# Optimization experiments

Measured on AMD Instinct MI355X. Metric: run time of the kernel, lower is better.

Reference implementation:

```python
import jax, jax.numpy as jnp
import numpy as np

B, LQ, LC, LN, D, H = 4, 1024, 1024, 1024, 1024, 16
HD = D // H
LS_INIT = 1e-4
RES_MAX = 10.0
EPS = 1e-5


def layernorm(x, g, b):
    mu = jnp.mean(x, axis=-1, keepdims=True)
    var = jnp.var(x, axis=-1, keepdims=True)
    return (x - mu) * jax.lax.rsqrt(var + EPS) * g + b


def setup_inputs() -> dict:
    key = jax.random.key(0)
    ks = jax.random.split(key, 12)
    s = 0.02
    return {
        "tight_tokens": jax.random.normal(ks[0], (B, LQ, D), jnp.float32),
        "context_tokens": jax.random.normal(ks[1], (B, LC, D), jnp.float32),
        "neighborhood_tokens": jax.random.normal(ks[2], (B, LN, D), jnp.float32),
        "ln_q_g": jnp.ones((D,), jnp.float32), "ln_q_b": jnp.zeros((D,), jnp.float32),
        "ln_kv_g": jnp.ones((D,), jnp.float32), "ln_kv_b": jnp.zeros((D,), jnp.float32),
        "in_proj_w": jax.random.normal(ks[3], (3 * D, D), jnp.float32) * s,
        "in_proj_b": jnp.zeros((3 * D,), jnp.float32),
        "out_proj_w": jax.random.normal(ks[4], (D, D), jnp.float32) * s,
        "out_proj_b": jnp.zeros((D,), jnp.float32),
        "cross_gamma": jnp.full((D,), LS_INIT, jnp.float32),
        "ln_f_g": jnp.ones((D,), jnp.float32), "ln_f_b": jnp.zeros((D,), jnp.float32),
        "w1": jax.random.normal(ks[5], (4 * D, D), jnp.float32) * s,
        "b1": jnp.zeros((4 * D,), jnp.float32),
        "w2": jax.random.normal(ks[6], (D, 4 * D), jnp.float32) * s,
        "b2": jnp.zeros((D,), jnp.float32),
        "ffn_gamma": jnp.full((D,), LS_INIT, jnp.float32),
    }


def reference(tight_tokens, context_tokens, neighborhood_tokens,
              ln_q_g, ln_q_b, ln_kv_g, ln_kv_b,
              in_proj_w, in_proj_b, out_proj_w, out_proj_b, cross_gamma,
              ln_f_g, ln_f_b, w1, b1, w2, b2, ffn_gamma):
    kv = jnp.concatenate([context_tokens, neighborhood_tokens], axis=1)  # [B, LKV, D]
    q_in = layernorm(tight_tokens, ln_q_g, ln_q_b)
    kv_in = layernorm(kv, ln_kv_g, ln_kv_b)

    wq, wk, wv = jnp.split(in_proj_w, 3, axis=0)
    bq, bk, bv = jnp.split(in_proj_b, 3, axis=0)
    q = (q_in @ wq.T + bq).reshape(B, LQ, H, HD)
    k = (kv_in @ wk.T + bk).reshape(B, -1, H, HD)
    v = (kv_in @ wv.T + bv).reshape(B, -1, H, HD)

    scores = jnp.einsum('bqhd,bkhd->bhqk', q, k) / jnp.sqrt(jnp.float32(HD))
    attn = jax.nn.softmax(scores, axis=-1)  # [B, H, LQ, LKV]
    ctx = jnp.einsum('bhqk,bkhd->bqhd', attn, v).reshape(B, LQ, D)
    attn_out = ctx @ out_proj_w.T + out_proj_b

    cg = jnp.clip(cross_gamma, -RES_MAX, RES_MAX)
    x = tight_tokens + attn_out * cg

    h = layernorm(x, ln_f_g, ln_f_b)
    h = jax.nn.gelu(h @ w1.T + b1, approximate=False) @ w2.T + b2
    fg = jnp.clip(ffn_gamma, -RES_MAX, RES_MAX)
    x = x + h * fg

    return x, attn.mean(axis=1)
```

## Files before the change

kernel.cpp:

```cpp
#include <hip/hip_runtime.h>
#include <math.h>

typedef unsigned short u16;
typedef __attribute__((ext_vector_type(8))) short bf16x8;
typedef __attribute__((ext_vector_type(4))) float f32x4;

#define MFMA16(a,b,c) __builtin_amdgcn_mfma_f32_16x16x32_bf16(a,b,c,0,0,0)

__device__ __forceinline__ u16 f2bf(float f){
  union { float f; unsigned int u; } x; x.f = f;
  unsigned int r = x.u + 0x7fffu + ((x.u >> 16) & 1u);
  return (u16)(r >> 16);
}

__device__ __forceinline__ void gload16(const void* g, void* lds){
  __builtin_amdgcn_global_load_lds(
    (const __attribute__((address_space(1))) unsigned int*)g,
    (__attribute__((address_space(3))) unsigned int*)lds, 16, 0, 0);
}

__global__ __launch_bounds__(256) void cvt_weights(
    const float* __restrict__ wqkv, const float* __restrict__ wo,
    const float* __restrict__ w1, const float* __restrict__ w2,
    u16* __restrict__ o0, u16* __restrict__ o1,
    u16* __restrict__ o2, u16* __restrict__ o3)
{
  int idx = blockIdx.x * 256 + threadIdx.x;
  const float* src; u16* dst;
  if (idx < 786432)                    { src = wqkv; dst = o0; }
  else if ((idx -= 786432) < 262144)   { src = wo;   dst = o1; }
  else if ((idx -= 262144) < 1048576)  { src = w1;   dst = o2; }
  else { idx -= 1048576;                 src = w2;   dst = o3; }
  float4 v = ((const float4*)src)[idx];
  short4 o;
  o.x = (short)f2bf(v.x); o.y = (short)f2bf(v.y);
  o.z = (short)f2bf(v.z); o.w = (short)f2bf(v.w);
  ((short4*)dst)[idx] = o;
}

template<int MODE>
__global__ __launch_bounds__(256) void ln_kernel(
    const float* __restrict__ s0, const float* __restrict__ s1,
    const float* __restrict__ g, const float* __restrict__ be,
    u16* __restrict__ out)
{
  int row = blockIdx.x, t = threadIdx.x;
  const float* src;
  if (MODE == 1) {
    int b = row >> 11, p = row & 2047;
    src = (p < 1024) ? s0 + ((long)(b*1024 + p))*1024
                     : s1 + ((long)(b*1024 + p - 1024))*1024;
  } else {
    src = s0 + (long)row * 1024;
  }
  float4 v = ((const float4*)src)[t];
  float s  = v.x + v.y + v.z + v.w;
  float ss = v.x*v.x + v.y*v.y + v.z*v.z + v.w*v.w;
  #pragma unroll
  for (int m = 1; m < 64; m <<= 1) { s += __shfl_xor(s, m); ss += __shfl_xor(ss, m); }
  __shared__ float red[8];
  int l = t & 63, w = t >> 6;
  if (l == 0) { red[w*2] = s; red[w*2+1] = ss; }
  __syncthreads();
  s  = red[0] + red[2] + red[4] + red[6];
  ss = red[1] + red[3] + red[5] + red[7];
  float mean = s * (1.0f/1024.0f);
  float var  = ss * (1.0f/1024.0f) - mean*mean;
  float rstd = rsqrtf(var + 1e-5f);
  float4 gv = ((const float4*)g)[t];
  float4 bv = ((const float4*)be)[t];
  short4 o;
  o.x = (short)f2bf((v.x-mean)*rstd*gv.x + bv.x);
  o.y = (short)f2bf((v.y-mean)*rstd*gv.y + bv.y);
  o.z = (short)f2bf((v.z-mean)*rstd*gv.z + bv.z);
  o.w = (short)f2bf((v.w-mean)*rstd*gv.w + bv.w);
  *(short4*)(out + (long)row*1024 + t*4) = o;
}

template<int EPI, int BM>
__global__ __launch_bounds__(256,2) void gemm_bt(
    const u16* __restrict__ A, const u16* __restrict__ Bt,
    int M, int N, int K,
    const float* __restrict__ bias,
    const float* __restrict__ gamma,
    const float* __restrict__ resid,
    float* __restrict__ outf,
    u16* __restrict__ outb0, u16* __restrict__ outb1)
{
  constexpr int MI = BM / 32;
  __shared__ __align__(16) u16 at[2][BM*64];
  __shared__ __align__(16) u16 bt[2][128*64];
  int nwg = gridDim.x;
  int bidx = (blockIdx.x & 7) * (nwg >> 3) + (blockIdx.x >> 3);
  int nb = N >> 7;
  int tm = bidx / nb, tn = bidx % nb;
  int m0 = tm * BM, n0 = tn << 7;
  int t = threadIdx.x, l = t & 63, w = t >> 6;
  int wr = (w >> 1) * (BM/2), wc = (w & 1) * 64;
  int fr = l & 15, fq = l >> 4;
  f32x4 acc[MI][4] = {};
  int rr = t >> 3;
  int cb = (t & 7) << 4;
  const char* Ab = (const char*)A;
  const char* Bp = (const char*)Bt;
  long ld = (long)K * 2;

#define G_STAGE(s, kt) do {                                                        \
    _Pragma("unroll")                                                              \
    for (int c = 0; c < MI; c++) {                                                 \
      int row = c*32 + rr;                                                         \
      gload16(Ab + (long)(m0 + row)*ld + (long)(kt)*2 + (cb ^ ((row & 7) << 4)),   \
              (char*)at[s] + c*4096 + w*1024);                                     \
    }                                                                              \
    _Pragma("unroll")                                                              \
    for (int c = 0; c < 4; c++) {                                                  \
      int row = c*32 + rr;                                                         \
      gload16(Bp + (long)(n0 + row)*ld + (long)(kt)*2 + (cb ^ ((row & 7) << 4)),   \
              (char*)bt[s] + c*4096 + w*1024);                                     \
    }                                                                              \
  } while (0)

  G_STAGE(0, 0);
  __syncthreads();
  int cur = 0;
  for (int kt = 0; kt < K; kt += 64) {
    if (kt + 64 < K) G_STAGE(cur ^ 1, kt + 64);
    #pragma unroll
    for (int ka = 0; ka < 2; ka++) {
      bf16x8 af[MI], bfv[4];
      #pragma unroll
      for (int i = 0; i < MI; i++) {
        int ra = wr + i*16 + fr;
        af[i] = *(const bf16x8*)((const char*)at[cur] + ra*128 + ((ka*64 + fq*16) ^ ((ra & 7) << 4)));
      }
      #pragma unroll
      for (int j = 0; j < 4; j++) {
        int rb = wc + j*16 + fr;
        bfv[j] = *(const bf16x8*)((const char*)bt[cur] + rb*128 + ((ka*64 + fq*16) ^ ((rb & 7) << 4)));
      }
      #pragma unroll
      for (int i = 0; i < MI; i++)
        #pragma unroll
        for (int j = 0; j < 4; j++)
          acc[i][j] = MFMA16(af[i], bfv[j], acc[i][j]);
    }
    __syncthreads();
    cur ^= 1;
  }
#undef G_STAGE
  #pragma unroll
  for (int i = 0; i < MI; i++) {
    #pragma unroll
    for (int j = 0; j < 4; j++) {
      #pragma unroll
      for (int r = 0; r < 4; r++) {
        int row = m0 + wr + i*16 + fq*4 + r;
        int col = n0 + wc + j*16 + fr;
        float v = acc[i][j][r];
        if constexpr (EPI == 0) {
          float qv = (v + bias[col]) * 0.18033688011112042f;
          int b = row >> 10, lq = row & 1023, h = col >> 6, hd = col & 63;
          outb0[(((long)(b*16 + h)) << 16) + (lq << 6) + hd] = f2bf(qv);
        } else if constexpr (EPI == 2) {
          float gs = gamma[col]; gs = fminf(fmaxf(gs, -10.f), 10.f);
          long idx = (long)row*1024 + col;
          outf[idx] = resid[idx] + (v + bias[col]) * gs;
        } else if constexpr (EPI == 3) {
          float u = v + bias[col];
          float ge = 0.5f * u * (1.0f + erff(u * 0.70710678118654752f));
          outb0[(long)row*4096 + col] = f2bf(ge);
        } else {
          float gs = gamma[col]; gs = fminf(fmaxf(gs, -10.f), 10.f);
          long idx = (long)row*1024 + col;
          outf[idx] = resid[idx] + (v + bias[col]) * gs;
        }
      }
    }
  }
}

template<int EPI>
__global__ __launch_bounds__(512, 2) void gemm256(
    const u16* __restrict__ A, const u16* __restrict__ Bt,
    int M, int N, int K,
    const float* __restrict__ bias,
    u16* __restrict__ outb0, u16* __restrict__ outb1)
{
  __shared__ __align__(16) u16 As[2][256*64];
  __shared__ __align__(16) u16 Bs[2][256*64];
  int nwg = gridDim.x;
  int bidx = (blockIdx.x & 7) * (nwg >> 3) + (blockIdx.x >> 3);
  int nb = N >> 8;
  int tm = bidx / nb, tn = bidx % nb;
  int m0 = tm << 8, n0 = tn << 8;
  int t = threadIdx.x, l = t & 63, w = t >> 6;
  int wm = w >> 2, wn = w & 3;
  int fr = l & 15, fq = l >> 4;
  int sr = t >> 3;
  int scb = (t & 7) << 4;
  int s7 = (sr & 7) << 4;
  const char* Ab = (const char*)A;
  const char* Bp = (const char*)Bt;
  long ld = (long)K * 2;

#define STAGE_AQ(slot, kt, q) do {                                               \
    int grow = (sr < 32) ? ((q)*32 + sr) : (128 + (q)*32 + sr - 32);             \
    int abase = (w < 4) ? ((q)*32 + w*8) : (128 + (q)*32 + (w - 4)*8);           \
    gload16(Ab + (long)(m0 + grow)*ld + (long)(kt)*2 + (scb ^ s7),               \
            (char*)As[slot] + abase*128);                                        \
  } while (0)
#define STAGE_BH(slot, kt, h) do {                                               \
    int r0 = (h)*128 + sr;                                                       \
    gload16(Bp + (long)(n0 + r0)*ld + (long)(kt)*2 + (scb ^ s7),                 \
            (char*)Bs[slot] + ((h)*128 + w*8)*128);                              \
    gload16(Bp + (long)(n0 + r0 + 64)*ld + (long)(kt)*2 + (scb ^ s7),            \
            (char*)Bs[slot] + ((h)*128 + 64 + w*8)*128);                         \
  } while (0)

  f32x4 acc[8][4] = {};
  int NT = K >> 6;

  STAGE_BH(0, 0, 0); STAGE_BH(0, 0, 1);
  STAGE_AQ(0, 0, 0); STAGE_AQ(0, 0, 1); STAGE_AQ(0, 0, 2); STAGE_AQ(0, 0, 3);
  STAGE_BH(1, 64, 0); STAGE_BH(1, 64, 1);
  asm volatile("s_waitcnt vmcnt(4)" ::: "memory");
  __builtin_amdgcn_s_barrier();
  asm volatile("" ::: "memory");

#define MFMA_PHASE(mibase)                                                       \
    __builtin_amdgcn_s_setprio(1);                                               \
    _Pragma("unroll")                                                            \
    for (int nj = 0; nj < 4; nj++) {                                             \
      acc[(mibase)][nj]   = MFMA16(a00, bfr[nj][0], acc[(mibase)][nj]);          \
      acc[(mibase)][nj]   = MFMA16(a01, bfr[nj][1], acc[(mibase)][nj]);          \
      acc[(mibase)+1][nj] = MFMA16(a10, bfr[nj][0], acc[(mibase)+1][nj]);        \
      acc[(mibase)+1][nj] = MFMA16(a11, bfr[nj][1], acc[(mibase)+1][nj]);        \
    }                                                                            \
    __builtin_amdgcn_s_setprio(0);

#define READ_A(p)                                                                \
    int r0_ = wm*128 + (2*(p))*16 + fr;                                          \
    int r1_ = r0_ + 16;                                                          \
    bf16x8 a00 = *(const bf16x8*)(Ab_s + r0_*128 + ((fq*16) ^ ((r0_ & 7) << 4)));        \
    bf16x8 a01 = *(const bf16x8*)(Ab_s + r0_*128 + ((64 + fq*16) ^ ((r0_ & 7) << 4)));   \
    bf16x8 a10 = *(const bf16x8*)(Ab_s + r1_*128 + ((fq*16) ^ ((r1_ & 7) << 4)));        \
    bf16x8 a11 = *(const bf16x8*)(Ab_s + r1_*128 + ((64 + fq*16) ^ ((r1_ & 7) << 4)));

  for (int tt = 0; tt < NT; tt++) {
    int s = tt & 1;
    const char* Ab_s = (const char*)As[s];
    const char* Bb_s = (const char*)Bs[s];
    int kt1 = (tt + 1) << 6, kt2 = (tt + 2) << 6;
    bf16x8 bfr[4][2];
    {
      #pragma unroll
      for (int nj = 0; nj < 4; nj++) {
        int rb = wn*64 + nj*16 + fr;
        bfr[nj][0] = *(const bf16x8*)(Bb_s + rb*128 + ((fq*16) ^ ((rb & 7) << 4)));
        bfr[nj][1] = *(const bf16x8*)(Bb_s + rb*128 + ((64 + fq*16) ^ ((rb & 7) << 4)));
      }
      READ_A(0)
      if (tt + 1 < NT) { STAGE_AQ(s ^ 1, kt1, 0); STAGE_AQ(s ^ 1, kt1, 1); }
      asm volatile("s_waitcnt lgkmcnt(8)" ::: "memory");
      __builtin_amdgcn_s_barrier();
      asm volatile("s_waitcnt lgkmcnt(0)" ::: "memory");
      MFMA_PHASE(0)
      __builtin_amdgcn_s_barrier();
    }
    {
      READ_A(1)
      if (tt + 1 < NT) { STAGE_AQ(s ^ 1, kt1, 2); STAGE_AQ(s ^ 1, kt1, 3); }
      __builtin_amdgcn_s_barrier();
      asm volatile("s_waitcnt lgkmcnt(0)" ::: "memory");
      MFMA_PHASE(2)
      __builtin_amdgcn_s_barrier();
    }
    {
      READ_A(2)
      if (tt + 2 < NT) STAGE_BH(s, kt2, 0);
      __builtin_amdgcn_s_barrier();
      asm volatile("s_waitcnt lgkmcnt(0)" ::: "memory");
      MFMA_PHASE(4)
      __builtin_amdgcn_s_barrier();
    }
    {
      READ_A(3)
      if (tt + 2 < NT) STAGE_BH(s, kt2, 1);
      __builtin_amdgcn_s_barrier();
      asm volatile("s_waitcnt lgkmcnt(0)" ::: "memory");
      MFMA_PHASE(6)
      if (tt + 1 < NT) {
        if (tt + 2 < NT) { asm volatile("s_waitcnt vmcnt(4)" ::: "memory"); }
        else             { asm volatile("s_waitcnt vmcnt(0)" ::: "memory"); }
      }
      __builtin_amdgcn_s_barrier();
      asm volatile("" ::: "memory");
    }
  }
#undef READ_A
#undef MFMA_PHASE
#undef STAGE_AQ
#undef STAGE_BH

  #pragma unroll
  for (int mi = 0; mi < 8; mi++) {
    #pragma unroll
    for (int nj = 0; nj < 4; nj++) {
      #pragma unroll
      for (int r = 0; r < 4; r++) {
        int row = m0 + wm*128 + mi*16 + fq*4 + r;
        int col = n0 + wn*64 + nj*16 + fr;
        float v = acc[mi][nj][r];
        if constexpr (EPI == 1) {
          float u = v + bias[col];
          int b = row >> 11, p = row & 2047;
          if (col < 1024) {
            int h = col >> 6, hd = col & 63;
            outb0[(((long)((b*16 + h)*2048 + p)) << 6) + hd] = f2bf(u);
          } else {
            int c2 = col - 1024, h = c2 >> 6, hd = c2 & 63;
            outb1[(((long)((b*16 + h)*64 + hd)) << 11) + p] = f2bf(u);
          }
        } else {
          float u = v + bias[col];
          float ge = 0.5f * u * (1.0f + erff(u * 0.70710678118654752f));
          outb0[(long)row*4096 + col] = f2bf(ge);
        }
      }
    }
  }
}

__global__ __launch_bounds__(256, 3) void flash_fwd(
    const u16* __restrict__ q, const u16* __restrict__ k,
    const u16* __restrict__ vt, u16* __restrict__ ctx,
    float* __restrict__ ilout)
{
  __shared__ __align__(16) u16 ks[2][64*64];
  __shared__ __align__(16) u16 vs[2][64*64];
  __shared__ __align__(16) char ps[4*4096];
  int nwg = gridDim.x;
  int bid = (blockIdx.x & 7) * (nwg >> 3) + (blockIdx.x >> 3);
  int qt = bid & 7, h = (bid >> 3) & 15, b = bid >> 7;
  int q0 = qt << 7;
  int t = threadIdx.x, l = t & 63, w = t >> 6;
  int fr = l & 15, fq = l >> 4;
  const char* qb = (const char*)(q  + (((long)(b*16 + h)) << 16));
  const char* kb = (const char*)(k  + (((long)(b*16 + h)) << 17));
  const char* vb = (const char*)(vt + (((long)(b*16 + h)) << 17));
  char* psw = ps + w*4096;
  int rr = t >> 3;
  int sc = (t & 7) << 4;

  #pragma unroll
  for (int c = 0; c < 2; c++) {
    int row = c*32 + rr;
    gload16(kb + (long)row*128 + (sc ^ ((row & 7) << 4)), (char*)ks[0] + c*4096 + w*1024);
    gload16(vb + (long)row*4096 + (sc ^ ((row & 7) << 4)), (char*)vs[0] + c*4096 + w*1024);
  }
  {
    int qr = l >> 3;
    #pragma unroll
    for (int c = 0; c < 4; c++) {
      int row = c*8 + qr;
      gload16(qb + (long)(q0 + w*32 + row)*128 + (sc ^ ((row & 7) << 4)), psw + c*1024);
    }
  }
  asm volatile("s_waitcnt vmcnt(0)" ::: "memory");
  bf16x8 qf[2][2];
  #pragma unroll
  for (int rf = 0; rf < 2; rf++) {
    int row = rf*16 + fr;
    qf[rf][0] = *(const bf16x8*)(psw + row*128 + ((fq*16) ^ ((row & 7) << 4)));
    qf[rf][1] = *(const bf16x8*)(psw + row*128 + ((64 + fq*16) ^ ((row & 7) << 4)));
  }
  asm volatile("s_waitcnt lgkmcnt(0)" ::: "memory");
  __builtin_amdgcn_s_barrier();
  asm volatile("" ::: "memory");

  f32x4 cacc[2][4] = {};
  f32x4 lrun[2] = {{0.f,0.f,0.f,0.f},{0.f,0.f,0.f,0.f}};
  int cur = 0;
  for (int kt = 0; kt < 2048; kt += 64) {
    int notlast = (kt + 64 < 2048);
    if (notlast) {
      #pragma unroll
      for (int c = 0; c < 2; c++) {
        int row = c*32 + rr;
        gload16(vb + (long)row*4096 + (long)(kt + 64)*2 + (sc ^ ((row & 7) << 4)),
                (char*)vs[cur ^ 1] + c*4096 + w*1024);
        gload16(kb + (long)(kt + 64 + row)*128 + (sc ^ ((row & 7) << 4)),
                (char*)ks[cur ^ 1] + c*4096 + w*1024);
      }
    }
    __builtin_amdgcn_sched_barrier(0);
    const char* ksb = (const char*)ks[cur];
    f32x4 sf[2][4];
    __builtin_amdgcn_s_setprio(1);
    #pragma unroll
    for (int cf = 0; cf < 4; cf++) {
      int row = cf*16 + fr;
      bf16x8 kf0 = *(const bf16x8*)(ksb + row*128 + ((fq*16) ^ ((row & 7) << 4)));
      bf16x8 kf1 = *(const bf16x8*)(ksb + row*128 + ((64 + fq*16) ^ ((row & 7) << 4)));
      #pragma unroll
      for (int rf = 0; rf < 2; rf++) {
        f32x4 a = {};
        a = MFMA16(qf[rf][0], kf0, a);
        sf[rf][cf] = MFMA16(qf[rf][1], kf1, a);
      }
    }
    __builtin_amdgcn_s_setprio(0);
    #pragma unroll
    for (int rf = 0; rf < 2; rf++)
      #pragma unroll
      for (int cf = 0; cf < 4; cf++)
        #pragma unroll
        for (int r = 0; r < 4; r++) {
          float pv = exp2f(sf[rf][cf][r]);
          lrun[rf][r] += pv;
          union { float f; unsigned int u; } pu; pu.f = pv;
          int prow = rf*16 + fq*4 + r;
          *(u16*)(psw + prow*128 + (((cf*16 + fr) << 1) ^ ((prow & 7) << 4))) = (u16)(pu.u >> 16);
        }
    bf16x8 pa[2][2];
    #pragma unroll
    for (int rf = 0; rf < 2; rf++) {
      int row = rf*16 + fr;
      pa[rf][0] = *(const bf16x8*)(psw + row*128 + ((fq*16) ^ ((row & 7) << 4)));
      pa[rf][1] = *(const bf16x8*)(psw + row*128 + ((64 + fq*16) ^ ((row & 7) << 4)));
    }
    __builtin_amdgcn_s_setprio(1);
    #pragma unroll
    for (int cfd = 0; cfd < 4; cfd++) {
      int hd = cfd*16 + fr;
      bf16x8 vf0 = *(const bf16x8*)((const char*)vs[cur] + hd*128 + ((fq*16) ^ ((hd & 7) << 4)));
      bf16x8 vf1 = *(const bf16x8*)((const char*)vs[cur] + hd*128 + ((64 + fq*16) ^ ((hd & 7) << 4)));
      #pragma unroll
      for (int rf = 0; rf < 2; rf++) {
        cacc[rf][cfd] = MFMA16(pa[rf][0], vf0, cacc[rf][cfd]);
        cacc[rf][cfd] = MFMA16(pa[rf][1], vf1, cacc[rf][cfd]);
      }
    }
    __builtin_amdgcn_s_setprio(0);
    if (notlast) {
      asm volatile("s_waitcnt vmcnt(0)" ::: "memory");
      __builtin_amdgcn_s_barrier();
      asm volatile("" ::: "memory");
    }
    cur ^= 1;
  }
  #pragma unroll
  for (int rf = 0; rf < 2; rf++) {
    float il4[4];
    #pragma unroll
    for (int r = 0; r < 4; r++) {
      float s = lrun[rf][r];
      #pragma unroll
      for (int msk = 1; msk < 16; msk <<= 1) s += __shfl_xor(s, msk, 16);
      il4[r] = 1.0f / s;
    }
    #pragma unroll
    for (int cf = 0; cf < 4; cf++)
      #pragma unroll
      for (int r = 0; r < 4; r++) {
        int row = q0 + w*32 + rf*16 + fq*4 + r;
        int col = h*64 + cf*16 + fr;
        ctx[(long)(b*1024 + row)*1024 + col] = f2bf(cacc[rf][cf][r] * il4[r]);
      }
    if (fr == 0) {
      #pragma unroll
      for (int r = 0; r < 4; r++) {
        int row = q0 + w*32 + rf*16 + fq*4 + r;
        long idx = (((long)(b*16 + h)) << 10) + row;
        ilout[idx] = il4[r];
      }
    }
  }
}

__global__ __launch_bounds__(256,2) void attn_mean(
    const u16* __restrict__ q, const u16* __restrict__ k,
    const float* __restrict__ il,
    float* __restrict__ out)
{
  __shared__ __align__(16) u16 qs[2][128*64];
  __shared__ __align__(16) u16 ks[2][128*64];
  __shared__ __align__(16) float ml[2][128];
  int nwg = gridDim.x;
  int bid = (blockIdx.x & 7) * (nwg >> 3) + (blockIdx.x >> 3);
  int kt = bid & 15, qt = (bid >> 4) & 7, b = bid >> 7;
  int q0 = qt << 7, k0 = kt << 7;
  int t = threadIdx.x, l = t & 63, w = t >> 6;
  int wr = (w >> 1) << 6, wc = (w & 1) << 6;
  int fr = l & 15, fq = l >> 4;
  int rr = t >> 3, cbb = (t & 7) << 4;
  const long bh = (long)b * 16;

#define AM_STAGE(hh, s) do {                                                        \
    const char* qb_ = (const char*)(q + ((bh + (hh)) << 16)) + (long)q0*128;        \
    const char* kb_ = (const char*)(k + ((bh + (hh)) << 17)) + (long)k0*128;        \
    _Pragma("unroll")                                                               \
    for (int c = 0; c < 4; c++) {                                                   \
      int row = c*32 + rr;                                                          \
      int sw = cbb ^ ((row & 7) << 4);                                              \
      gload16(qb_ + (long)row*128 + sw, (char*)qs[s] + c*4096 + w*1024);            \
      gload16(kb_ + (long)row*128 + sw, (char*)ks[s] + c*4096 + w*1024);            \
    }                                                                               \
    if (w == 0 && l < 32) {                                                         \
      gload16((const char*)(il + ((bh + (hh)) << 10) + q0) + l*16, (char*)ml[s]);   \
    }                                                                               \
  } while (0)

  AM_STAGE(0, 0);
  asm volatile("s_waitcnt vmcnt(0)" ::: "memory");
  __builtin_amdgcn_s_barrier();
  asm volatile("" ::: "memory");

  f32x4 macc[4][4] = {};
  for (int h = 0; h < 16; h++) {
    int cur = h & 1;
    if (h < 15) AM_STAGE(h + 1, cur ^ 1);
    const char* qsb = (const char*)qs[cur];
    const char* ksb = (const char*)ks[cur];
    const float* mlb = ml[cur];
    f32x4 ir4[4];
    #pragma unroll
    for (int i = 0; i < 4; i++)
      ir4[i] = *(const f32x4*)(mlb + wr + i*16 + fq*4);
    bf16x8 af[4][2], bf[4][2];
    #pragma unroll
    for (int i = 0; i < 4; i++) {
      int ra = wr + i*16 + fr;
      int rb = wc + i*16 + fr;
      af[i][0] = *(const bf16x8*)(qsb + ra*128 + ((fq*16) ^ ((ra & 7) << 4)));
      af[i][1] = *(const bf16x8*)(qsb + ra*128 + ((64 + fq*16) ^ ((ra & 7) << 4)));
      bf[i][0] = *(const bf16x8*)(ksb + rb*128 + ((fq*16) ^ ((rb & 7) << 4)));
      bf[i][1] = *(const bf16x8*)(ksb + rb*128 + ((64 + fq*16) ^ ((rb & 7) << 4)));
    }
    #pragma unroll
    for (int j = 0; j < 4; j++) {
      f32x4 sf[4];
      __builtin_amdgcn_s_setprio(1);
      #pragma unroll
      for (int i = 0; i < 4; i++) {
        f32x4 a = MFMA16(af[i][0], bf[j][0], {});
        sf[i] = MFMA16(af[i][1], bf[j][1], a);
      }
      __builtin_amdgcn_s_setprio(0);
      #pragma unroll
      for (int i = 0; i < 4; i++)
        #pragma unroll
        for (int r = 0; r < 4; r++)
          macc[i][j][r] += exp2f(sf[i][r]) * ir4[i][r];
    }
    asm volatile("s_waitcnt vmcnt(0)" ::: "memory");
    __builtin_amdgcn_s_barrier();
    asm volatile("" ::: "memory");
  }
#undef AM_STAGE
  #pragma unroll
  for (int i = 0; i < 4; i++)
    #pragma unroll
    for (int j = 0; j < 4; j++)
      #pragma unroll
      for (int r = 0; r < 4; r++) {
        int row = q0 + wr + i*16 + fq*4 + r;
        int col = k0 + wc + j*16 + fr;
        out[((long)(b*1024 + row) << 11) + col] = macc[i][j][r] * 0.0625f;
      }
}

extern "C" void kernel_launch(void* const* d_in, const int* in_sizes, int n_in,
                              void* d_out, int out_size, void* d_ws, size_t ws_size,
                              hipStream_t stream)
{
  (void)in_sizes; (void)n_in; (void)out_size; (void)ws_size;
  const float* tight = (const float*)d_in[0];
  const float* ctxt  = (const float*)d_in[1];
  const float* nbh   = (const float*)d_in[2];
  const float* lnqg  = (const float*)d_in[3];
  const float* lnqb  = (const float*)d_in[4];
  const float* lnkg  = (const float*)d_in[5];
  const float* lnkb  = (const float*)d_in[6];
  const float* wqkv  = (const float*)d_in[7];
  const float* bqkv  = (const float*)d_in[8];
  const float* wo    = (const float*)d_in[9];
  const float* bo    = (const float*)d_in[10];
  const float* cg    = (const float*)d_in[11];
  const float* lnfg  = (const float*)d_in[12];
  const float* lnfb  = (const float*)d_in[13];
  const float* w1    = (const float*)d_in[14];
  const float* b1    = (const float*)d_in[15];
  const float* w2    = (const float*)d_in[16];
  const float* b2    = (const float*)d_in[17];
  const float* fg    = (const float*)d_in[18];

  char* p = (char*)d_ws;
  u16* wqkv_bf = (u16*)p; p += 3072L*1024*2;
  u16* wo_bf   = (u16*)p; p += 1024L*1024*2;
  u16* w1_bf   = (u16*)p; p += 4096L*1024*2;
  u16* w2_bf   = (u16*)p; p += 1024L*4096*2;
  u16* qin_bf  = (u16*)p; p += 4096L*1024*2;
  u16* kvin_bf = (u16*)p; p += 8192L*1024*2;
  u16* q_bf    = (u16*)p; p += 4L*16*1024*64*2;
  u16* k_bf    = (u16*)p; p += 4L*16*2048*64*2;
  u16* vt_bf   = (u16*)p; p += 4L*16*64*2048*2;
  u16* ctx_bf  = (u16*)p; p += 4096L*1024*2;
  float* il_f  = (float*)p; p += 4L*16*1024*4;
  float* x_f   = (float*)p; p += 4096L*1024*4;
  u16* hln_bf  = (u16*)p; p += 4096L*1024*2;
  u16* gelu_bf = (u16*)p; p += 4096L*4096*2;

  float* x_out    = (float*)d_out;
  float* mean_out = x_out + 4194304;

  cvt_weights<<<12288, 256, 0, stream>>>(wqkv, wo, w1, w2, wqkv_bf, wo_bf, w1_bf, w2_bf);
  ln_kernel<0><<<4096, 256, 0, stream>>>(tight, nullptr, lnqg, lnqb, qin_bf);
  ln_kernel<1><<<8192, 256, 0, stream>>>(ctxt, nbh, lnkg, lnkb, kvin_bf);
  gemm_bt<0,64><<<512, 256, 0, stream>>>(qin_bf, wqkv_bf, 4096, 1024, 1024,
                                      bqkv, nullptr, nullptr, nullptr, q_bf, nullptr);
  gemm256<1><<<256, 512, 0, stream>>>(kvin_bf, wqkv_bf + 1024L*1024, 8192, 2048, 1024,
                                      bqkv + 1024, k_bf, vt_bf);
  flash_fwd<<<512, 256, 0, stream>>>(q_bf, k_bf, vt_bf, ctx_bf, il_f);
  attn_mean<<<512, 256, 0, stream>>>(q_bf, k_bf, il_f, mean_out);
  gemm_bt<2,64><<<512, 256, 0, stream>>>(ctx_bf, wo_bf, 4096, 1024, 1024,
                                      bo, cg, tight, x_f, nullptr, nullptr);
  ln_kernel<0><<<4096, 256, 0, stream>>>(x_f, nullptr, lnfg, lnfb, hln_bf);
  gemm256<3><<<256, 512, 0, stream>>>(hln_bf, w1_bf, 4096, 4096, 1024,
                                      b1, gelu_bf, nullptr);
  gemm_bt<4,64><<<512, 256, 0, stream>>>(gelu_bf, w2_bf, 4096, 1024, 4096,
                                      b2, fg, x_f, x_out, nullptr, nullptr);
}
```

Measured before the change: 360.6 us.

## Merge Q and KV projections into one launch; co-schedule attn-mean with out-proj

Replaces the separate Q-projection gemm_bt and KV gemm256 launches with a single 320-block gemm256_qkv that routes each block to the KV or Q tile by index. It also fuses the attention-mean kernel and the output-projection GEMM into one post_attn launch whose blocks branch between the two independent jobs. The aim is to cut launch overhead and tail underutilisation by filling the GPU with concurrent independent work. The cost is heterogeneous blocks inside one grid, with possible load imbalance, and a shared LDS footprint sized for the larger branch, which may lower occupancy.

```diff
diff --git a/kernel.cpp b/kernel.cpp
--- a/kernel.cpp
+++ b/kernel.cpp
@@ -157,15 +157,7 @@
         int row = m0 + wr + i*16 + fq*4 + r;
         int col = n0 + wc + j*16 + fr;
         float v = acc[i][j][r];
-        if constexpr (EPI == 0) {
-          float qv = (v + bias[col]) * 0.18033688011112042f;
-          int b = row >> 10, lq = row & 1023, h = col >> 6, hd = col & 63;
-          outb0[(((long)(b*16 + h)) << 16) + (lq << 6) + hd] = f2bf(qv);
-        } else if constexpr (EPI == 2) {
-          float gs = gamma[col]; gs = fminf(fmaxf(gs, -10.f), 10.f);
-          long idx = (long)row*1024 + col;
-          outf[idx] = resid[idx] + (v + bias[col]) * gs;
-        } else if constexpr (EPI == 3) {
+        if constexpr (EPI == 3) {
           float u = v + bias[col];
           float ge = 0.5f * u * (1.0f + erff(u * 0.70710678118654752f));
           outb0[(long)row*4096 + col] = f2bf(ge);
@@ -179,12 +171,102 @@
   }
 }
 
-template<int EPI>
-__global__ __launch_bounds__(512, 2) void gemm256(
+#define STAGE_AQ(slot, kt, q) do {                                               \
+    int grow = (sr < 32) ? ((q)*32 + sr) : (128 + (q)*32 + sr - 32);             \
+    int abase = (w < 4) ? ((q)*32 + w*8) : (128 + (q)*32 + (w - 4)*8);           \
+    gload16(Ab + (long)(m0 + grow)*ld + (long)(kt)*2 + (scb ^ s7),               \
+            (char*)As[slot] + abase*128);                                        \
+  } while (0)
+#define STAGE_BH(slot, kt, h) do {                                               \
+    int r0 = (h)*128 + sr;                                                       \
+    gload16(Bp + (long)(n0 + r0)*ld + (long)(kt)*2 + (scb ^ s7),                 \
+            (char*)Bs[slot] + ((h)*128 + w*8)*128);                              \
+    gload16(Bp + (long)(n0 + r0 + 64)*ld + (long)(kt)*2 + (scb ^ s7),            \
+            (char*)Bs[slot] + ((h)*128 + 64 + w*8)*128);                         \
+  } while (0)
+#define MFMA_PHASE(mibase)                                                       \
+    __builtin_amdgcn_s_setprio(1);                                               \
+    _Pragma("unroll")                                                            \
+    for (int nj = 0; nj < 4; nj++) {                                             \
+      acc[(mibase)][nj]   = MFMA16(a00, bfr[nj][0], acc[(mibase)][nj]);          \
+      acc[(mibase)][nj]   = MFMA16(a01, bfr[nj][1], acc[(mibase)][nj]);          \
+      acc[(mibase)+1][nj] = MFMA16(a10, bfr[nj][0], acc[(mibase)+1][nj]);        \
+      acc[(mibase)+1][nj] = MFMA16(a11, bfr[nj][1], acc[(mibase)+1][nj]);        \
+    }                                                                            \
+    __builtin_amdgcn_s_setprio(0);
+#define READ_A(p)                                                                \
+    int r0_ = wm*128 + (2*(p))*16 + fr;                                          \
+    int r1_ = r0_ + 16;                                                          \
+    bf16x8 a00 = *(const bf16x8*)(Ab_s + r0_*128 + ((fq*16) ^ ((r0_ & 7) << 4)));        \
+    bf16x8 a01 = *(const bf16x8*)(Ab_s + r0_*128 + ((64 + fq*16) ^ ((r0_ & 7) << 4)));   \
+    bf16x8 a10 = *(const bf16x8*)(Ab_s + r1_*128 + ((fq*16) ^ ((r1_ & 7) << 4)));        \
+    bf16x8 a11 = *(const bf16x8*)(Ab_s + r1_*128 + ((64 + fq*16) ^ ((r1_ & 7) << 4)));
+
+#define GEMM256_BODY                                                             \
+  f32x4 acc[8][4] = {};                                                          \
+  STAGE_BH(0, 0, 0); STAGE_BH(0, 0, 1);                                          \
+  STAGE_AQ(0, 0, 0); STAGE_AQ(0, 0, 1); STAGE_AQ(0, 0, 2); STAGE_AQ(0, 0, 3);    \
+  STAGE_BH(1, 64, 0); STAGE_BH(1, 64, 1);                                        \
+  asm volatile("s_waitcnt vmcnt(4)" ::: "memory");                               \
+  __builtin_amdgcn_s_barrier();                                                  \
+  asm volatile("" ::: "memory");                                                 \
+  for (int tt = 0; tt < NT; tt++) {                                              \
+    int s = tt & 1;                                                              \
+    const char* Ab_s = (const char*)As[s];                                       \
+    const char* Bb_s = (const char*)Bs[s];                                       \
+    int kt1 = (tt + 1) << 6, kt2 = (tt + 2) << 6;                                \
+    bf16x8 bfr[4][2];                                                            \
+    {                                                                            \
+      _Pragma("unroll")                                                          \
+      for (int nj = 0; nj < 4; nj++) {                                           \
+        int rb = wn*64 + nj*16 + fr;                                             \
+        bfr[nj][0] = *(const bf16x8*)(Bb_s + rb*128 + ((fq*16) ^ ((rb & 7) << 4)));      \
+        bfr[nj][1] = *(const bf16x8*)(Bb_s + rb*128 + ((64 + fq*16) ^ ((rb & 7) << 4))); \
+      }                                                                          \
+      READ_A(0)                                                                  \
+      if (tt + 1 < NT) { STAGE_AQ(s ^ 1, kt1, 0); STAGE_AQ(s ^ 1, kt1, 1); }     \
+      asm volatile("s_waitcnt lgkmcnt(8)" ::: "memory");                         \
+      __builtin_amdgcn_s_barrier();                                              \
+      asm volatile("s_waitcnt lgkmcnt(0)" ::: "memory");                         \
+      MFMA_PHASE(0)                                                              \
+      __builtin_amdgcn_s_barrier();                                              \
+    }                                                                            \
+    {                                                                            \
+      READ_A(1)                                                                  \
+      if (tt + 1 < NT) { STAGE_AQ(s ^ 1, kt1, 2); STAGE_AQ(s ^ 1, kt1, 3); }     \
+      __builtin_amdgcn_s_barrier();                                              \
+      asm volatile("s_waitcnt lgkmcnt(0)" ::: "memory");                         \
+      MFMA_PHASE(2)                                                              \
+      __builtin_amdgcn_s_barrier();                                              \
+    }                                                                            \
+    {                                                                            \
+      READ_A(2)                                                                  \
+      if (tt + 2 < NT) STAGE_BH(s, kt2, 0);                                      \
+      __builtin_amdgcn_s_barrier();                                              \
+      asm volatile("s_waitcnt lgkmcnt(0)" ::: "memory");                         \
+      MFMA_PHASE(4)                                                              \
+      __builtin_amdgcn_s_barrier();                                              \
+    }                                                                            \
+    {                                                                            \
+      READ_A(3)                                                                  \
+      if (tt + 2 < NT) STAGE_BH(s, kt2, 1);                                      \
+      __builtin_amdgcn_s_barrier();                                              \
+      asm volatile("s_waitcnt lgkmcnt(0)" ::: "memory");                         \
+      MFMA_PHASE(6)                                                              \
+      if (tt + 1 < NT) {                                                         \
+        if (tt + 2 < NT) { asm volatile("s_waitcnt vmcnt(4)" ::: "memory"); }    \
+        else             { asm volatile("s_waitcnt vmcnt(0)" ::: "memory"); }    \
+      }                                                                          \
+      __builtin_amdgcn_s_barrier();                                              \
+      asm volatile("" ::: "memory");                                             \
+    }                                                                            \
+  }
+
+__global__ __launch_bounds__(512, 2) void gemm256_ffn1(
     const u16* __restrict__ A, const u16* __restrict__ Bt,
     int M, int N, int K,
     const float* __restrict__ bias,
-    u16* __restrict__ outb0, u16* __restrict__ outb1)
+    u16* __restrict__ outb0)
 {
   __shared__ __align__(16) u16 As[2][256*64];
   __shared__ __align__(16) u16 Bs[2][256*64];
@@ -202,133 +284,74 @@
   const char* Ab = (const char*)A;
   const char* Bp = (const char*)Bt;
   long ld = (long)K * 2;
-
-#define STAGE_AQ(slot, kt, q) do {                                               \
-    int grow = (sr < 32) ? ((q)*32 + sr) : (128 + (q)*32 + sr - 32);             \
-    int abase = (w < 4) ? ((q)*32 + w*8) : (128 + (q)*32 + (w - 4)*8);           \
-    gload16(Ab + (long)(m0 + grow)*ld + (long)(kt)*2 + (scb ^ s7),               \
-            (char*)As[slot] + abase*128);                                        \
-  } while (0)
-#define STAGE_BH(slot, kt, h) do {                                               \
-    int r0 = (h)*128 + sr;                                                       \
-    gload16(Bp + (long)(n0 + r0)*ld + (long)(kt)*2 + (scb ^ s7),                 \
-            (char*)Bs[slot] + ((h)*128 + w*8)*128);                              \
-    gload16(Bp + (long)(n0 + r0 + 64)*ld + (long)(kt)*2 + (scb ^ s7),            \
-            (char*)Bs[slot] + ((h)*128 + 64 + w*8)*128);                         \
-  } while (0)
-
-  f32x4 acc[8][4] = {};
   int NT = K >> 6;
-
-  STAGE_BH(0, 0, 0); STAGE_BH(0, 0, 1);
-  STAGE_AQ(0, 0, 0); STAGE_AQ(0, 0, 1); STAGE_AQ(0, 0, 2); STAGE_AQ(0, 0, 3);
-  STAGE_BH(1, 64, 0); STAGE_BH(1, 64, 1);
-  asm volatile("s_waitcnt vmcnt(4)" ::: "memory");
-  __builtin_amdgcn_s_barrier();
-  asm volatile("" ::: "memory");
-
-#define MFMA_PHASE(mibase)                                                       \
-    __builtin_amdgcn_s_setprio(1);                                               \
-    _Pragma("unroll")                                                            \
-    for (int nj = 0; nj < 4; nj++) {                                             \
-      acc[(mibase)][nj]   = MFMA16(a00, bfr[nj][0], acc[(mibase)][nj]);          \
-      acc[(mibase)][nj]   = MFMA16(a01, bfr[nj][1], acc[(mibase)][nj]);          \
-      acc[(mibase)+1][nj] = MFMA16(a10, bfr[nj][0], acc[(mibase)+1][nj]);        \
-      acc[(mibase)+1][nj] = MFMA16(a11, bfr[nj][1], acc[(mibase)+1][nj]);        \
-    }                                                                            \
-    __builtin_amdgcn_s_setprio(0);
-
-#define READ_A(p)                                                                \
-    int r0_ = wm*128 + (2*(p))*16 + fr;                                          \
-    int r1_ = r0_ + 16;                                                          \
-    bf16x8 a00 = *(const bf16x8*)(Ab_s + r0_*128 + ((fq*16) ^ ((r0_ & 7) << 4)));        \
-    bf16x8 a01 = *(const bf16x8*)(Ab_s + r0_*128 + ((64 + fq*16) ^ ((r0_ & 7) << 4)));   \
-    bf16x8 a10 = *(const bf16x8*)(Ab_s + r1_*128 + ((fq*16) ^ ((r1_ & 7) << 4)));        \
-    bf16x8 a11 = *(const bf16x8*)(Ab_s + r1_*128 + ((64 + fq*16) ^ ((r1_ & 7) << 4)));
-
-  for (int tt = 0; tt < NT; tt++) {
-    int s = tt & 1;
-    const char* Ab_s = (const char*)As[s];
-    const char* Bb_s = (const char*)Bs[s];
-    int kt1 = (tt + 1) << 6, kt2 = (tt + 2) << 6;
-    bf16x8 bfr[4][2];
-    {
-      #pragma unroll
-      for (int nj = 0; nj < 4; nj++) {
-        int rb = wn*64 + nj*16 + fr;
-        bfr[nj][0] = *(const bf16x8*)(Bb_s + rb*128 + ((fq*16) ^ ((rb & 7) << 4)));
-        bfr[nj][1] = *(const bf16x8*)(Bb_s + rb*128 + ((64 + fq*16) ^ ((rb & 7) << 4)));
-      }
-      READ_A(0)
-      if (tt + 1 < NT) { STAGE_AQ(s ^ 1, kt1, 0); STAGE_AQ(s ^ 1, kt1, 1); }
-      asm volatile("s_waitcnt lgkmcnt(8)" ::: "memory");
-      __builtin_amdgcn_s_barrier();
-      asm volatile("s_waitcnt lgkmcnt(0)" ::: "memory");
-      MFMA_PHASE(0)
-      __builtin_amdgcn_s_barrier();
-    }
-    {
-      READ_A(1)
-      if (tt + 1 < NT) { STAGE_AQ(s ^ 1, kt1, 2); STAGE_AQ(s ^ 1, kt1, 3); }
-      __builtin_amdgcn_s_barrier();
-      asm volatile("s_waitcnt lgkmcnt(0)" ::: "memory");
-      MFMA_PHASE(2)
-      __builtin_amdgcn_s_barrier();
-    }
-    {
-      READ_A(2)
-      if (tt + 2 < NT) STAGE_BH(s, kt2, 0);
-      __builtin_amdgcn_s_barrier();
-      asm volatile("s_waitcnt lgkmcnt(0)" ::: "memory");
-      MFMA_PHASE(4)
-      __builtin_amdgcn_s_barrier();
-    }
-    {
-      READ_A(3)
-      if (tt + 2 < NT) STAGE_BH(s, kt2, 1);
-      __builtin_amdgcn_s_barrier();
-      asm volatile("s_waitcnt lgkmcnt(0)" ::: "memory");
-      MFMA_PHASE(6)
-      if (tt + 1 < NT) {
-        if (tt + 2 < NT) { asm volatile("s_waitcnt vmcnt(4)" ::: "memory"); }
-        else             { asm volatile("s_waitcnt vmcnt(0)" ::: "memory"); }
-      }
-      __builtin_amdgcn_s_barrier();
-      asm volatile("" ::: "memory");
-    }
-  }
-#undef READ_A
-#undef MFMA_PHASE
-#undef STAGE_AQ
-#undef STAGE_BH
-
+  GEMM256_BODY
   #pragma unroll
-  for (int mi = 0; mi < 8; mi++) {
-    #pragma unroll
-    for (int nj = 0; nj < 4; nj++) {
+  for (int mi = 0; mi < 8; mi++)
+    #pragma unroll
+    for (int nj = 0; nj < 4; nj++)
+      #pragma unroll
+      for (int r = 0; r < 4; r++) {
+        int row = m0 + wm*128 + mi*16 + fq*4 + r;
+        int col = n0 + wn*64 + nj*16 + fr;
+        float u = acc[mi][nj][r] + bias[col];
+        float ge = 0.5f * u * (1.0f + erff(u * 0.70710678118654752f));
+        outb0[(long)row*4096 + col] = f2bf(ge);
+      }
+}
+
+__global__ __launch_bounds__(512, 2) void gemm256_qkv(
+    const u16* __restrict__ qin, const u16* __restrict__ kvin,
+    const u16* __restrict__ wqkv_b,
+    const float* __restrict__ bias,
+    u16* __restrict__ qo, u16* __restrict__ ko, u16* __restrict__ vto)
+{
+  __shared__ __align__(16) u16 As[2][256*64];
+  __shared__ __align__(16) u16 Bs[2][256*64];
+  int nwg = gridDim.x;
+  int bidx = (blockIdx.x & 7) * (nwg >> 3) + (blockIdx.x >> 3);
+  int iskv = (bidx < 256);
+  int tm, tn;
+  const char* Ab; const char* Bp;
+  if (iskv) { tm = bidx >> 3; tn = bidx & 7;
+              Ab = (const char*)kvin; Bp = (const char*)(wqkv_b + 1024L*1024); }
+  else      { int i = bidx - 256; tm = i >> 2; tn = i & 3;
+              Ab = (const char*)qin;  Bp = (const char*)wqkv_b; }
+  int m0 = tm << 8, n0 = tn << 8;
+  int t = threadIdx.x, l = t & 63, w = t >> 6;
+  int wm = w >> 2, wn = w & 3;
+  int fr = l & 15, fq = l >> 4;
+  int sr = t >> 3;
+  int scb = (t & 7) << 4;
+  int s7 = (sr & 7) << 4;
+  long ld = 2048;
+  int NT = 16;
+  GEMM256_BODY
+  #pragma unroll
+  for (int mi = 0; mi < 8; mi++)
+    #pragma unroll
+    for (int nj = 0; nj < 4; nj++)
       #pragma unroll
       for (int r = 0; r < 4; r++) {
         int row = m0 + wm*128 + mi*16 + fq*4 + r;
         int col = n0 + wn*64 + nj*16 + fr;
         float v = acc[mi][nj][r];
-        if constexpr (EPI == 1) {
-          float u = v + bias[col];
+        if (iskv) {
+          float u = v + bias[1024 + col];
           int b = row >> 11, p = row & 2047;
           if (col < 1024) {
             int h = col >> 6, hd = col & 63;
-            outb0[(((long)((b*16 + h)*2048 + p)) << 6) + hd] = f2bf(u);
+            ko[(((long)((b*16 + h)*2048 + p)) << 6) + hd] = f2bf(u);
           } else {
             int c2 = col - 1024, h = c2 >> 6, hd = c2 & 63;
-            outb1[(((long)((b*16 + h)*64 + hd)) << 11) + p] = f2bf(u);
+            vto[(((long)((b*16 + h)*64 + hd)) << 11) + p] = f2bf(u);
           }
         } else {
-          float u = v + bias[col];
-          float ge = 0.5f * u * (1.0f + erff(u * 0.70710678118654752f));
-          outb0[(long)row*4096 + col] = f2bf(ge);
+          float qv = (v + bias[col]) * 0.18033688011112042f;
+          int b = row >> 10, lq = row & 1023, h = col >> 6, hd = col & 63;
+          qo[(((long)(b*16 + h)) << 16) + (lq << 6) + hd] = f2bf(qv);
         }
       }
-    }
-  }
 }
 
 __global__ __launch_bounds__(256, 3) void flash_fwd(
@@ -478,23 +501,29 @@
   }
 }
 
-__global__ __launch_bounds__(256,2) void attn_mean(
+__global__ __launch_bounds__(256, 2) void post_attn(
     const u16* __restrict__ q, const u16* __restrict__ k,
-    const float* __restrict__ il,
-    float* __restrict__ out)
+    const float* __restrict__ il, float* __restrict__ mean_out,
+    const u16* __restrict__ ctx, const u16* __restrict__ wo_b,
+    const float* __restrict__ bo, const float* __restrict__ cg,
+    const float* __restrict__ tight, float* __restrict__ x_f)
 {
-  __shared__ __align__(16) u16 qs[2][128*64];
-  __shared__ __align__(16) u16 ks[2][128*64];
-  __shared__ __align__(16) float ml[2][128];
+  __shared__ __align__(16) char smem[66560];
   int nwg = gridDim.x;
-  int bid = (blockIdx.x & 7) * (nwg >> 3) + (blockIdx.x >> 3);
-  int kt = bid & 15, qt = (bid >> 4) & 7, b = bid >> 7;
-  int q0 = qt << 7, k0 = kt << 7;
+  int bidx = (blockIdx.x & 7) * (nwg >> 3) + (blockIdx.x >> 3);
   int t = threadIdx.x, l = t & 63, w = t >> 6;
-  int wr = (w >> 1) << 6, wc = (w & 1) << 6;
   int fr = l & 15, fq = l >> 4;
-  int rr = t >> 3, cbb = (t & 7) << 4;
-  const long bh = (long)b * 16;
+
+  if ((bidx & 1) == 0) {
+    int bid = bidx >> 1;
+    u16 (*qs)[128*64] = (u16 (*)[128*64])smem;
+    u16 (*ks)[128*64] = (u16 (*)[128*64])(smem + 32768);
+    float (*ml)[128]  = (float (*)[128])(smem + 65536);
+    int kt = bid & 15, qt = (bid >> 4) & 7, b = bid >> 7;
+    int q0 = qt << 7, k0 = kt << 7;
+    int wr = (w >> 1) << 6, wc = (w & 1) << 6;
+    int rr = t >> 3, cbb = (t & 7) << 4;
+    const long bh = (long)b * 16;
 
 #define AM_STAGE(hh, s) do {                                                        \
     const char* qb_ = (const char*)(q + ((bh + (hh)) << 16)) + (long)q0*128;        \
@@ -511,63 +540,133 @@
     }                                                                               \
   } while (0)
 
-  AM_STAGE(0, 0);
-  asm volatile("s_waitcnt vmcnt(0)" ::: "memory");
-  __builtin_amdgcn_s_barrier();
-  asm volatile("" ::: "memory");
-
-  f32x4 macc[4][4] = {};
-  for (int h = 0; h < 16; h++) {
-    int cur = h & 1;
-    if (h < 15) AM_STAGE(h + 1, cur ^ 1);
-    const char* qsb = (const char*)qs[cur];
-    const char* ksb = (const char*)ks[cur];
-    const float* mlb = ml[cur];
-    f32x4 ir4[4];
-    #pragma unroll
-    for (int i = 0; i < 4; i++)
-      ir4[i] = *(const f32x4*)(mlb + wr + i*16 + fq*4);
-    bf16x8 af[4][2], bf[4][2];
-    #pragma unroll
-    for (int i = 0; i < 4; i++) {
-      int ra = wr + i*16 + fr;
-      int rb = wc + i*16 + fr;
-      af[i][0] = *(const bf16x8*)(qsb + ra*128 + ((fq*16) ^ ((ra & 7) << 4)));
-      af[i][1] = *(const bf16x8*)(qsb + ra*128 + ((64 + fq*16) ^ ((ra & 7) << 4)));
-      bf[i][0] = *(const bf16x8*)(ksb + rb*128 + ((fq*16) ^ ((rb & 7) << 4)));
-      bf[i][1] = *(const bf16x8*)(ksb + rb*128 + ((64 + fq*16) ^ ((rb & 7) << 4)));
-    }
-    #pragma unroll
-    for (int j = 0; j < 4; j++) {
-      f32x4 sf[4];
-      __builtin_amdgcn_s_setprio(1);
-      #pragma unroll
-      for (int i = 0; i < 4; i++) {
-        f32x4 a = MFMA16(af[i][0], bf[j][0], {});
-        sf[i] = MFMA16(af[i][1], bf[j][1], a);
-      }
-      __builtin_amdgcn_s_setprio(0);
-      #pragma unroll
-      for (int i = 0; i < 4; i++)
-        #pragma unroll
-        for (int r = 0; r < 4; r++)
-          macc[i][j][r] += exp2f(sf[i][r]) * ir4[i][r];
-    }
+    AM_STAGE(0, 0);
     asm volatile("s_waitcnt vmcnt(0)" ::: "memory");
     __builtin_amdgcn_s_barrier();
     asm volatile("" ::: "memory");
-  }
+
+    f32x4 macc[4][4] = {};
+    for (int h = 0; h < 16; h++) {
+      int cur = h & 1;
+      if (h < 15) AM_STAGE(h + 1, cur ^ 1);
+      const char* qsb = (const char*)qs[cur];
+      const char* ksb = (const char*)ks[cur];
+      const float* mlb = ml[cur];
+      f32x4 ir4[4];
+      #pragma unroll
+      for (int i = 0; i < 4; i++)
+        ir4[i] = *(const f32x4*)(mlb + wr + i*16 + fq*4);
+      bf16x8 af[4][2], bf[4][2];
+      #pragma unroll
+      for (int i = 0; i < 4; i++) {
+        int ra = wr + i*16 + fr;
+        int rb = wc + i*16 + fr;
+        af[i][0] = *(const bf16x8*)(qsb + ra*128 + ((fq*16) ^ ((ra & 7) << 4)));
+        af[i][1] = *(const bf16x8*)(qsb + ra*128 + ((64 + fq*16) ^ ((ra & 7) << 4)));
+        bf[i][0] = *(const bf16x8*)(ksb + rb*128 + ((fq*16) ^ ((rb & 7) << 4)));
+        bf[i][1] = *(const bf16x8*)(ksb + rb*128 + ((64 + fq*16) ^ ((rb & 7) << 4)));
+      }
+      #pragma unroll
+      for (int j = 0; j < 4; j++) {
+        f32x4 sf[4];
+        __builtin_amdgcn_s_setprio(1);
+        #pragma unroll
+        for (int i = 0; i < 4; i++) {
+          f32x4 a = MFMA16(af[i][0], bf[j][0], {});
+          sf[i] = MFMA16(af[i][1], bf[j][1], a);
+        }
+        __builtin_amdgcn_s_setprio(0);
+        #pragma unroll
+        for (int i = 0; i < 4; i++)
+          #pragma unroll
+          for (int r = 0; r < 4; r++)
+            macc[i][j][r] += exp2f(sf[i][r]) * ir4[i][r];
+      }
+      asm volatile("s_waitcnt vmcnt(0)" ::: "memory");
+      __builtin_amdgcn_s_barrier();
+      asm volatile("" ::: "memory");
+    }
 #undef AM_STAGE
-  #pragma unroll
-  for (int i = 0; i < 4; i++)
-    #pragma unroll
-    for (int j = 0; j < 4; j++)
-      #pragma unroll
-      for (int r = 0; r < 4; r++) {
-        int row = q0 + wr + i*16 + fq*4 + r;
-        int col = k0 + wc + j*16 + fr;
-        out[((long)(b*1024 + row) << 11) + col] = macc[i][j][r] * 0.0625f;
-      }
+    #pragma unroll
+    for (int i = 0; i < 4; i++)
+      #pragma unroll
+      for (int j = 0; j < 4; j++)
+        #pragma unroll
+        for (int r = 0; r < 4; r++) {
+          int row = q0 + wr + i*16 + fq*4 + r;
+          int col = k0 + wc + j*16 + fr;
+          mean_out[((long)(b*1024 + row) << 11) + col] = macc[i][j][r] * 0.0625f;
+        }
+  } else {
+    int bid = bidx >> 1;
+    u16 (*at)[64*64]  = (u16 (*)[64*64])smem;
+    u16 (*bt)[128*64] = (u16 (*)[128*64])(smem + 16384);
+    int tm = bid >> 3, tn = bid & 7;
+    int m0 = tm << 6, n0 = tn << 7;
+    int wr = (w >> 1) * 32, wc = (w & 1) * 64;
+    f32x4 acc[2][4] = {};
+    int rr = t >> 3;
+    int cb = (t & 7) << 4;
+    const char* Ab = (const char*)ctx;
+    const char* Bp = (const char*)wo_b;
+    long ld = 2048;
+
+#define O_STAGE(s, kt) do {                                                        \
+    _Pragma("unroll")                                                              \
+    for (int c = 0; c < 2; c++) {                                                  \
+      int row = c*32 + rr;                                                         \
+      gload16(Ab + (long)(m0 + row)*ld + (long)(kt)*2 + (cb ^ ((row & 7) << 4)),   \
+              (char*)at[s] + c*4096 + w*1024);                                     \
+    }                                                                              \
+    _Pragma("unroll")                                                              \
+    for (int c = 0; c < 4; c++) {                                                  \
+      int row = c*32 + rr;                                                         \
+      gload16(Bp + (long)(n0 + row)*ld + (long)(kt)*2 + (cb ^ ((row & 7) << 4)),   \
+              (char*)bt[s] + c*4096 + w*1024);                                     \
+    }                                                                              \
+  } while (0)
+
+    O_STAGE(0, 0);
+    __syncthreads();
+    int cur = 0;
+    for (int kt = 0; kt < 1024; kt += 64) {
+      if (kt + 64 < 1024) O_STAGE(cur ^ 1, kt + 64);
+      #pragma unroll
+      for (int ka = 0; ka < 2; ka++) {
+        bf16x8 af[2], bfv[4];
+        #pragma unroll
+        for (int i = 0; i < 2; i++) {
+          int ra = wr + i*16 + fr;
+          af[i] = *(const bf16x8*)((const char*)at[cur] + ra*128 + ((ka*64 + fq*16) ^ ((ra & 7) << 4)));
+        }
+        #pragma unroll
+        for (int j = 0; j < 4; j++) {
+          int rb = wc + j*16 + fr;
+          bfv[j] = *(const bf16x8*)((const char*)bt[cur] + rb*128 + ((ka*64 + fq*16) ^ ((rb & 7) << 4)));
+        }
+        #pragma unroll
+        for (int i = 0; i < 2; i++)
+          #pragma unroll
+          for (int j = 0; j < 4; j++)
+            acc[i][j] = MFMA16(af[i], bfv[j], acc[i][j]);
+      }
+      __syncthreads();
+      cur ^= 1;
+    }
+#undef O_STAGE
+    #pragma unroll
+    for (int i = 0; i < 2; i++)
+      #pragma unroll
+      for (int j = 0; j < 4; j++)
+        #pragma unroll
+        for (int r = 0; r < 4; r++) {
+          int row = m0 + wr + i*16 + fq*4 + r;
+          int col = n0 + wc + j*16 + fr;
+          float gs = cg[col]; gs = fminf(fmaxf(gs, -10.f), 10.f);
+          long idx = (long)row*1024 + col;
+          x_f[idx] = tight[idx] + (acc[i][j][r] + bo[col]) * gs;
+        }
+  }
 }
 
 extern "C" void kernel_launch(void* const* d_in, const int* in_sizes, int n_in,
@@ -617,17 +716,14 @@
   cvt_weights<<<12288, 256, 0, stream>>>(wqkv, wo, w1, w2, wqkv_bf, wo_bf, w1_bf, w2_bf);
   ln_kernel<0><<<4096, 256, 0, stream>>>(tight, nullptr, lnqg, lnqb, qin_bf);
   ln_kernel<1><<<8192, 256, 0, stream>>>(ctxt, nbh, lnkg, lnkb, kvin_bf);
-  gemm_bt<0,64><<<512, 256, 0, stream>>>(qin_bf, wqkv_bf, 4096, 1024, 1024,
-                                      bqkv, nullptr, nullptr, nullptr, q_bf, nullptr);
-  gemm256<1><<<256, 512, 0, stream>>>(kvin_bf, wqkv_bf + 1024L*1024, 8192, 2048, 1024,
-                                      bqkv + 1024, k_bf, vt_bf);
+  gemm256_qkv<<<320, 512, 0, stream>>>(qin_bf, kvin_bf, wqkv_bf, bqkv,
+                                       q_bf, k_bf, vt_bf);
   flash_fwd<<<512, 256, 0, stream>>>(q_bf, k_bf, vt_bf, ctx_bf, il_f);
-  attn_mean<<<512, 256, 0, stream>>>(q_bf, k_bf, il_f, mean_out);
-  gemm_bt<2,64><<<512, 256, 0, stream>>>(ctx_bf, wo_bf, 4096, 1024, 1024,
-                                      bo, cg, tight, x_f, nullptr, nullptr);
+  post_attn<<<1024, 256, 0, stream>>>(q_bf, k_bf, il_f, mean_out,
+                                      ctx_bf, wo_bf, bo, cg, tight, x_f);
   ln_kernel<0><<<4096, 256, 0, stream>>>(x_f, nullptr, lnfg, lnfb, hln_bf);
-  gemm256<3><<<256, 512, 0, stream>>>(hln_bf, w1_bf, 4096, 4096, 1024,
-                                      b1, gelu_bf, nullptr);
+  gemm256_ffn1<<<256, 512, 0, stream>>>(hln_bf, w1_bf, 4096, 4096, 1024,
+                                        b1, gelu_bf);
   gemm_bt<4,64><<<512, 256, 0, stream>>>(gelu_bf, w2_bf, 4096, 1024, 4096,
                                       b2, fg, x_f, x_out, nullptr, nullptr);
 }
```

Result: slower. 418.9 us (+16.2%).
